# Performance work log

Hardware: AMD Instinct MI355X
Metric: run time of the kernel (lower is better)

The kernel has to match this reference:

```python
import jax, jax.numpy as jnp
import numpy as np

N = 50000        # nodes per node type (user, item)
D_IN = 256       # node_in_dim
D_REL = 64       # rel_in_dim
K = 8            # num_heads
D_OUT = 32       # node_out_dim (per head); K*D_OUT = 256
D_RELOUT = 32    # rel_out_dim (per head)
E = 300000       # edges per relation direction
SLOPE = 0.2

# relations: 0 = user-rates->item, 1 = item-rated-by->user,
#            2 = user-clicks->item, 3 = item-clicked-by->user
STYPE = [0, 1, 0, 1]   # 0=user, 1=item
DTYPE = [1, 0, 1, 0]
REV   = [1, 0, 3, 2]
GROUP = [[0, 2], [1, 3], [0, 2], [1, 3]]  # relations sharing this relation's dtype


def setup_inputs() -> dict:
    key = jax.random.key(0)
    ks = jax.random.split(key, 16)
    feats = jax.random.normal(ks[0], (4, N, D_IN), jnp.float32)
    rel_feats = jax.random.normal(ks[1], (4, D_REL), jnp.float32)
    src_rates = jax.random.randint(ks[2], (E,), 0, N, jnp.int32)
    dst_rates = jax.random.randint(ks[3], (E,), 0, N, jnp.int32)
    src_clicks = jax.random.randint(ks[4], (E,), 0, N, jnp.int32)
    dst_clicks = jax.random.randint(ks[5], (E,), 0, N, jnp.int32)
    s = 0.05
    W_node = s * jax.random.normal(ks[6], (2, D_IN, K * D_OUT), jnp.float32)          # fc_node per ntype (no bias)
    Wr = s * jax.random.normal(ks[7], (4, D_REL, 2 * K * D_OUT), jnp.float32)         # fc_rel per etype (no bias)
    Wres = s * jax.random.normal(ks[8], (2, D_IN, K * D_OUT), jnp.float32)            # fc_res per ntype
    bres = s * jax.random.normal(ks[9], (2, K * D_OUT), jnp.float32)
    resw = jax.random.uniform(ks[10], (2,), jnp.float32)                              # res_weight per ntype
    rel_attn = s * jax.random.normal(ks[11], (4, K, D_OUT), jnp.float32)              # rel_attn per etype
    Wupd = s * jax.random.normal(ks[12], (4, D_REL, K * D_RELOUT), jnp.float32)       # fc_upd per etype
    bupd = s * jax.random.normal(ks[13], (4, K * D_RELOUT), jnp.float32)
    return dict(feats=feats, rel_feats=rel_feats, src_rates=src_rates, dst_rates=dst_rates,
                src_clicks=src_clicks, dst_clicks=dst_clicks, W_node=W_node, Wr=Wr,
                Wres=Wres, bres=bres, resw=resw, rel_attn=rel_attn, Wupd=Wupd, bupd=bupd)


def _leaky(x):
    return jnp.where(x >= 0, x, SLOPE * x)


def _rel_graph_conv(hs, hd, attn, src, dst):
    """GAT-style conv for one relation. hs,hd: (N,K,D_OUT); attn: (K,2*D_OUT)."""
    el = (hs * attn[:, :D_OUT]).sum(-1)                    # (N_src, K)
    er = (hd * attn[:, D_OUT:]).sum(-1)                    # (N_dst, K)
    e = _leaky(el[src] + er[dst])                          # (E, K)
    # edge softmax grouped by destination node
    m = jax.ops.segment_max(e, dst, num_segments=N)        # (N, K)
    m = jnp.where(jnp.isfinite(m), m, 0.0)                 # nodes with no incoming edges
    ex = jnp.exp(e - m[dst])
    z = jax.ops.segment_sum(ex, dst, num_segments=N)
    a = ex / z[dst]                                        # (E, K)
    msg = hs[src] * a[:, :, None]                          # (E, K, D_OUT)
    out = jax.ops.segment_sum(msg, dst, num_segments=N)    # (N, K, D_OUT)
    return jax.nn.relu(out.reshape(N, K * D_OUT))


def reference(feats, rel_feats, src_rates, dst_rates, src_clicks, dst_clicks,
              W_node, Wr, Wres, bres, resw, rel_attn, Wupd, bupd):
    srcs = [src_rates, dst_rates, src_clicks, dst_clicks]
    dsts = [dst_rates, src_rates, dst_clicks, src_clicks]

    node_rel = []
    for r in range(4):
        # feat_src = feats of stype nodes (stored under the reverse relation); feat_dst under r
        hs = (feats[REV[r]] @ W_node[STYPE[r]]).reshape(N, K, D_OUT)
        hd = (feats[r] @ W_node[DTYPE[r]]).reshape(N, K, D_OUT)
        attn = (rel_feats[r] @ Wr[r]).reshape(K, 2 * D_OUT)
        conv = _rel_graph_conv(hs, hd, attn, srcs[r], dsts[r])
        # residual per destination node type
        alpha = jax.nn.sigmoid(resw[DTYPE[r]])
        inherit = feats[r] @ Wres[DTYPE[r]] + bres[DTYPE[r]]
        node_rel.append(alpha * conv + (1.0 - alpha) * inherit)

    # cross-relation attention per relation (over relations sharing the same dtype)
    out_feats = []
    for r in range(4):
        h = jnp.stack([node_rel[i] for i in GROUP[r]], 0).reshape(len(GROUP[r]), N, K, D_OUT)
        scores = (rel_attn[r] * h).sum(-1, keepdims=True)           # (R, N, K, 1)
        w = jax.nn.softmax(_leaky(scores), axis=0)
        out_feats.append((w * h).sum(0).reshape(N, K * D_OUT))
    out_nodes = jnp.stack(out_feats, 0)                             # (4, N, K*D_OUT)

    rel_out = jnp.einsum('rd,rdo->ro', rel_feats, Wupd) + bupd      # (4, K*D_RELOUT)
    return out_nodes, rel_out
```

## Files before the change

### kernel.cpp

```cpp
#include <hip/hip_runtime.h>

typedef unsigned short u16;
typedef __bf16 bf16x8 __attribute__((ext_vector_type(8)));
typedef float f32x4 __attribute__((ext_vector_type(4)));

#define N_NODES 50000
#define N_EDGES 300000
#define NP      12800000
#define NE8     400000

#define WP_OFF    0L
#define ATTN_OFF  524288L
#define ALPHA_OFF 532480L
#define P_OFF     532544L
#define EL_OFF    102932544L
#define ER_OFF    109332544L
#define CNT_OFF   115732544L
#define CUR_OFF   116532544L
#define ROW_OFF   117332544L
#define BS_OFF    118132560L
#define COL_OFF   118135696L

__device__ __forceinline__ float bf2f(u16 u){
  union { unsigned int i; float f; } v; v.i = ((unsigned int)u) << 16; return v.f;
}
__device__ __forceinline__ u16 f2bf(float f){
  union { float f; unsigned int i; } v; v.f = f;
  unsigned int x = v.i;
  x += 0x7fffu + ((x >> 16) & 1u);
  return (u16)(x >> 16);
}
__device__ __forceinline__ float leaky(float x){ return x >= 0.f ? x : 0.2f * x; }

__global__ void small_k(const float* __restrict__ rel_feats, const float* __restrict__ Wr,
                        const float* __restrict__ Wupd, const float* __restrict__ bupd,
                        const float* __restrict__ resw,
                        float* __restrict__ attn, float* __restrict__ alpha,
                        float* __restrict__ out_tail){
  int r = blockIdx.x, t = threadIdx.x;
  for (int j = t; j < 512; j += 256){
    float s = 0.f;
    for (int d = 0; d < 64; ++d)
      s += rel_feats[r*64 + d] * Wr[(r*64 + d)*512 + j];
    attn[r*512 + j] = s;
  }
  {
    float s = 0.f;
    for (int d = 0; d < 64; ++d)
      s += rel_feats[r*64 + d] * Wupd[(r*64 + d)*256 + t];
    out_tail[r*256 + t] = s + bupd[r*256 + t];
  }
  if (r == 0 && t < 2) alpha[t] = 1.f / (1.f + __expf(-resw[t]));
}

__global__ void prepack_k(const float* __restrict__ Wn, const float* __restrict__ Wres,
                          u16* __restrict__ Wp){
  int tid = blockIdx.x*256 + threadIdx.x;
  int m = tid >> 16, rem = tid & 65535;
  int kt = rem >> 13, rem2 = rem & 8191;
  int n = rem2 >> 5, kk = rem2 & 31;
  const float* src = (m < 2) ? (Wn + m*65536) : (Wres + (m - 2)*65536);
  Wp[tid] = f2bf(src[(kt*32 + kk)*256 + n]);
}

__global__ __launch_bounds__(256, 2) void gemm_k(const float* __restrict__ A,
                                              const u16* __restrict__ Wpn, const u16* __restrict__ Wpr,
                                              const float* __restrict__ bias,
                                              const float* __restrict__ alpha_ws, int tix,
                                              u16* __restrict__ Pout, float* __restrict__ out,
                                              const float* __restrict__ attnL, const float* __restrict__ attnR,
                                              float* __restrict__ ELb, float* __restrict__ ERb){
  const int tid = threadIdx.x;
  const int lane = tid & 63, wave = tid >> 6;
  const int quad = lane >> 4, n0 = lane & 15;
  const int wrow = blockIdx.x*64;
  const int cbase = wave*64;
  f32x4 accn[4][4], accr[4][4];
#pragma unroll
  for (int f = 0; f < 4; ++f)
#pragma unroll
    for (int nt = 0; nt < 4; ++nt){
      accn[f][nt] = f32x4{0.f,0.f,0.f,0.f};
      accr[f][nt] = f32x4{0.f,0.f,0.f,0.f};
    }

  for (int kt = 0; kt < 8; ++kt){
    const u16* bpn = Wpn + kt*8192 + (cbase + n0)*32 + quad*8;
    const u16* bpr = Wpr + kt*8192 + (cbase + n0)*32 + quad*8;
    bf16x8 bn[4], br[4];
#pragma unroll
    for (int nt = 0; nt < 4; ++nt){
      bn[nt] = *(const bf16x8*)(bpn + nt*16*32);
      br[nt] = *(const bf16x8*)(bpr + nt*16*32);
    }
    union { bf16x8 v; u16 s[8]; } af[4];
#pragma unroll
    for (int f = 0; f < 4; ++f){
      int row = wrow + f*16 + n0;
      if (row < N_NODES){
        const float* ap = A + (size_t)row*256 + kt*32 + quad*8;
        f32x4 a0 = *(const f32x4*)ap;
        f32x4 a1 = *(const f32x4*)(ap + 4);
#pragma unroll
        for (int j = 0; j < 4; ++j){ af[f].s[j] = f2bf(a0[j]); af[f].s[4+j] = f2bf(a1[j]); }
      } else {
#pragma unroll
        for (int j = 0; j < 8; ++j) af[f].s[j] = 0;
      }
    }
#pragma unroll
    for (int f = 0; f < 4; ++f)
#pragma unroll
      for (int nt = 0; nt < 4; ++nt){
        accn[f][nt] = __builtin_amdgcn_mfma_f32_16x16x32_bf16(af[f].v, bn[nt], accn[f][nt], 0, 0, 0);
        accr[f][nt] = __builtin_amdgcn_mfma_f32_16x16x32_bf16(af[f].v, br[nt], accr[f][nt], 0, 0, 0);
      }
  }

  const float one_m_al = 1.f - alpha_ws[tix];
#pragma unroll
  for (int f = 0; f < 4; ++f)
#pragma unroll
    for (int nt = 0; nt < 4; ++nt){
      int col = cbase + nt*16 + n0;
      float b = bias[col];
#pragma unroll
      for (int reg = 0; reg < 4; ++reg){
        int row = wrow + f*16 + quad*4 + reg;
        if (row < N_NODES){
          out[(size_t)row*256 + col] = one_m_al * (accr[f][nt][reg] + b);
          Pout[(size_t)row*256 + col] = f2bf(accn[f][nt][reg]);
        }
      }
    }

  const int h0 = 2*wave, h1 = 2*wave + 1;
  const float aL00 = attnL[h0*64 + n0], aL01 = attnL[h0*64 + 16 + n0];
  const float aL10 = attnL[h1*64 + n0], aL11 = attnL[h1*64 + 16 + n0];
  const float aR00 = attnR[h0*64 + n0], aR01 = attnR[h0*64 + 16 + n0];
  const float aR10 = attnR[h1*64 + n0], aR11 = attnR[h1*64 + 16 + n0];
#pragma unroll
  for (int f = 0; f < 4; ++f){
#pragma unroll
    for (int reg = 0; reg < 4; ++reg){
      float e0 = accn[f][0][reg]*aL00 + accn[f][1][reg]*aL01;
      float e1 = accn[f][2][reg]*aL10 + accn[f][3][reg]*aL11;
      float r0 = accn[f][0][reg]*aR00 + accn[f][1][reg]*aR01;
      float r1 = accn[f][2][reg]*aR10 + accn[f][3][reg]*aR11;
      e0 += __shfl_xor(e0, 1); e0 += __shfl_xor(e0, 2); e0 += __shfl_xor(e0, 4); e0 += __shfl_xor(e0, 8);
      e1 += __shfl_xor(e1, 1); e1 += __shfl_xor(e1, 2); e1 += __shfl_xor(e1, 4); e1 += __shfl_xor(e1, 8);
      r0 += __shfl_xor(r0, 1); r0 += __shfl_xor(r0, 2); r0 += __shfl_xor(r0, 4); r0 += __shfl_xor(r0, 8);
      r1 += __shfl_xor(r1, 1); r1 += __shfl_xor(r1, 2); r1 += __shfl_xor(r1, 4); r1 += __shfl_xor(r1, 8);
      int row = wrow + f*16 + quad*4 + reg;
      if (row < N_NODES){
        if (n0 == 0)      ELb[row*8 + h0] = e0;
        else if (n0 == 1) ELb[row*8 + h1] = e1;
        else if (n0 == 2) ERb[row*8 + h0] = r0;
        else if (n0 == 3) ERb[row*8 + h1] = r1;
      }
    }
  }
}

__global__ void zero_k(int* __restrict__ p, int n){
  int i = blockIdx.x*256 + threadIdx.x; if (i < n) p[i] = 0;
}
__global__ void hist_k(const int* __restrict__ sr, const int* __restrict__ dr,
                       const int* __restrict__ sc, const int* __restrict__ dc,
                       int* __restrict__ counts){
  int r = blockIdx.y; int e = blockIdx.x*256 + threadIdx.x;
  if (e >= N_EDGES) return;
  const int* dst = (r == 0) ? dr : (r == 1) ? sr : (r == 2) ? dc : sc;
  atomicAdd(&counts[r*N_NODES + dst[e]], 1);
}
__global__ void scan1_k(const int* __restrict__ counts, int* __restrict__ rowptr,
                        int* __restrict__ bsums){
  int r = blockIdx.y; int i = blockIdx.x*256 + threadIdx.x;
  int lane = threadIdx.x & 63, wave = threadIdx.x >> 6;
  int v = (i < N_NODES) ? counts[r*N_NODES + i] : 0;
  int orig = v;
  for (int off = 1; off < 64; off <<= 1){ int t = __shfl_up(v, off); if (lane >= off) v += t; }
  __shared__ int wsum[4];
  if (lane == 63) wsum[wave] = v;
  __syncthreads();
  int add = 0;
  for (int w = 0; w < wave; ++w) add += wsum[w];
  v += add;
  if (i < N_NODES) rowptr[r*(N_NODES+1) + i] = v - orig;
  if (threadIdx.x == 255) bsums[r*196 + blockIdx.x] = v;
}
__global__ void scan2_k(int* __restrict__ bsums){
  int lane = threadIdx.x & 63, r = threadIdx.x >> 6;
  int carry = 0;
  for (int c = 0; c < 4; ++c){
    int i = c*64 + lane;
    int v = (i < 196) ? bsums[r*196 + i] : 0;
    int orig = v;
    for (int off = 1; off < 64; off <<= 1){ int t = __shfl_up(v, off); if (lane >= off) v += t; }
    int excl = v - orig + carry;
    if (i < 196) bsums[r*196 + i] = excl;
    carry += __shfl(v, 63);
  }
}
__global__ void scan3_k(const int* __restrict__ bsums, int* __restrict__ rowptr){
  int r = blockIdx.y; int i = blockIdx.x*256 + threadIdx.x;
  if (i < N_NODES) rowptr[r*(N_NODES+1) + i] += bsums[r*196 + blockIdx.x];
  if (i == N_NODES) rowptr[r*(N_NODES+1) + N_NODES] = N_EDGES;
}
__global__ void scatter_k(const int* __restrict__ sr, const int* __restrict__ dr,
                          const int* __restrict__ sc, const int* __restrict__ dc,
                          const int* __restrict__ rowptr, int* __restrict__ cur,
                          int* __restrict__ colsrc){
  int r = blockIdx.y; int e = blockIdx.x*256 + threadIdx.x;
  if (e >= N_EDGES) return;
  const int* dst = (r == 0) ? dr : (r == 1) ? sr : (r == 2) ? dc : sc;
  const int* src = (r == 0) ? sr : (r == 1) ? dr : (r == 2) ? sc : dc;
  int d = dst[e];
  int pos = rowptr[r*(N_NODES+1) + d] + atomicAdd(&cur[r*N_NODES + d], 1);
  colsrc[r*N_EDGES + pos] = src[e];
}

__global__ __launch_bounds__(256) void aggcross_k(
    const int* __restrict__ rowptr, const int* __restrict__ colsrc,
    const float* __restrict__ EL, const float* __restrict__ ER,
    const u16* __restrict__ P, const float* __restrict__ rel_attn,
    const float* __restrict__ alpha_ws, float* __restrict__ out){
  const int g = blockIdx.y;
  const int wave = threadIdx.x >> 6, lane = threadIdx.x & 63;
  const int n = blockIdx.x*4 + wave;
  if (n >= N_NODES) return;
  const int k0 = lane >> 3, j = lane & 7;
  const float al = alpha_ws[g ^ 1];
  f32x4 h[2];
#pragma unroll
  for (int which = 0; which < 2; ++which){
    const int r = g + which*2;
    const int rp0 = rowptr[r*(N_NODES+1) + n], rp1 = rowptr[r*(N_NODES+1) + n + 1];
    const float er = ER[(size_t)r*NE8 + n*8 + k0];
    const float* el = EL + (size_t)r*NE8;
    const int* cs = colsrc + r*N_EDGES;
    const u16* Ps = P + (size_t)(r ^ 1)*NP;

    float z = 0.f, a0 = 0.f, a1 = 0.f, a2 = 0.f, a3 = 0.f;
    for (int base = rp0; base < rp1; base += 8){
      const int cnt = rp1 - base;
      const int m = cnt < 8 ? cnt : 8;
      int sj = cs[base + (j < m ? j : 0)];
      float x = leaky(el[sj*8 + k0] + er);
      float p = (j < m) ? __expf(x - 10.f) : 0.f;
      ushort4 hv[8]; float pv[8];
#pragma unroll
      for (int t = 0; t < 8; ++t){
        if (t < m){
          int s = __shfl(sj, t);
          hv[t] = *(const ushort4*)(Ps + (size_t)s*256 + lane*4);
          pv[t] = __shfl(p, (lane & 56) | t);
        }
      }
#pragma unroll
      for (int t = 0; t < 8; ++t){
        if (t < m){
          float q = pv[t];
          z += q;
          a0 += q*bf2f(hv[t].x); a1 += q*bf2f(hv[t].y);
          a2 += q*bf2f(hv[t].z); a3 += q*bf2f(hv[t].w);
        }
      }
    }
    float inv = (rp1 > rp0) ? 1.f / z : 0.f;
    f32x4 inh = *(const f32x4*)(out + (size_t)r*NP + (size_t)n*256 + lane*4);
    h[which][0] = al * fmaxf(a0*inv, 0.f) + inh[0];
    h[which][1] = al * fmaxf(a1*inv, 0.f) + inh[1];
    h[which][2] = al * fmaxf(a2*inv, 0.f) + inh[2];
    h[which][3] = al * fmaxf(a3*inv, 0.f) + inh[3];
  }
#pragma unroll
  for (int which = 0; which < 2; ++which){
    int rr = g + which*2;
    const float* ra = rel_attn + rr*256 + k0*32 + j*4;
    float s0 = 0.f, s1 = 0.f;
#pragma unroll
    for (int jj = 0; jj < 4; ++jj){
      float a = ra[jj];
      s0 += a * h[0][jj]; s1 += a * h[1][jj];
    }
    s0 += __shfl_xor(s0, 1); s1 += __shfl_xor(s1, 1);
    s0 += __shfl_xor(s0, 2); s1 += __shfl_xor(s1, 2);
    s0 += __shfl_xor(s0, 4); s1 += __shfl_xor(s1, 4);
    float l0 = leaky(s0), l1 = leaky(s1);
    float mx = fmaxf(l0, l1);
    float e0 = __expf(l0 - mx), e1 = __expf(l1 - mx);
    float w0 = e0 / (e0 + e1), w1 = 1.f - w0;
    f32x4 o;
#pragma unroll
    for (int jj = 0; jj < 4; ++jj) o[jj] = w0*h[0][jj] + w1*h[1][jj];
    *(f32x4*)(out + ((size_t)rr*N_NODES + n)*256 + lane*4) = o;
  }
}

extern "C" void kernel_launch(void* const* d_in, const int* in_sizes, int n_in,
                              void* d_out, int out_size, void* d_ws, size_t ws_size,
                              hipStream_t stream) {
  (void)in_sizes; (void)n_in; (void)out_size; (void)ws_size;
  const float* feats      = (const float*)d_in[0];
  const float* rel_feats  = (const float*)d_in[1];
  const int*   src_rates  = (const int*)d_in[2];
  const int*   dst_rates  = (const int*)d_in[3];
  const int*   src_clicks = (const int*)d_in[4];
  const int*   dst_clicks = (const int*)d_in[5];
  const float* W_node     = (const float*)d_in[6];
  const float* Wr         = (const float*)d_in[7];
  const float* Wres       = (const float*)d_in[8];
  const float* bres       = (const float*)d_in[9];
  const float* resw       = (const float*)d_in[10];
  const float* rel_attn   = (const float*)d_in[11];
  const float* Wupd       = (const float*)d_in[12];
  const float* bupd       = (const float*)d_in[13];

  char* w = (char*)d_ws;
  u16*   Wp     = (u16*)(w + WP_OFF);
  float* attn   = (float*)(w + ATTN_OFF);
  float* alpha  = (float*)(w + ALPHA_OFF);
  u16*   P      = (u16*)(w + P_OFF);
  float* EL     = (float*)(w + EL_OFF);
  float* ER     = (float*)(w + ER_OFF);
  int*   counts = (int*)(w + CNT_OFF);
  int*   cur    = (int*)(w + CUR_OFF);
  int*   rowptr = (int*)(w + ROW_OFF);
  int*   bsums  = (int*)(w + BS_OFF);
  int*   colsrc = (int*)(w + COL_OFF);
  float* out    = (float*)d_out;

  static const int DT[4] = {1, 0, 1, 0};

  zero_k<<<1563, 256, 0, stream>>>(counts, 400000);
  small_k<<<4, 256, 0, stream>>>(rel_feats, Wr, Wupd, bupd, resw, attn, alpha,
                                 out + (size_t)4*NP);
  prepack_k<<<1024, 256, 0, stream>>>(W_node, Wres, Wp);

  hist_k<<<dim3(1172, 4), 256, 0, stream>>>(src_rates, dst_rates, src_clicks, dst_clicks, counts);
  scan1_k<<<dim3(196, 4), 256, 0, stream>>>(counts, rowptr, bsums);
  scan2_k<<<1, 256, 0, stream>>>(bsums);
  scan3_k<<<dim3(196, 4), 256, 0, stream>>>(bsums, rowptr);
  scatter_k<<<dim3(1172, 4), 256, 0, stream>>>(src_rates, dst_rates, src_clicks, dst_clicks,
                                               rowptr, cur, colsrc);

  for (int i = 0; i < 4; ++i)
    gemm_k<<<782, 256, 0, stream>>>(feats + (size_t)i*NP,
                                    Wp + DT[i]*65536, Wp + (2 + DT[i])*65536,
                                    bres + DT[i]*256, alpha, DT[i],
                                    P + (size_t)i*NP, out + (size_t)i*NP,
                                    attn + (i ^ 1)*512, attn + i*512 + 32,
                                    EL + (size_t)(i ^ 1)*NE8, ER + (size_t)i*NE8);

  aggcross_k<<<dim3(12500, 2), 256, 0, stream>>>(rowptr, colsrc, EL, ER, P,
                                                 rel_attn, alpha, out);
}
```

Baseline: 927.0 us.

## Merge per-relation GEMM launches into one grid and software-pipeline global loads

Replaces four separate gemm_k launches with one launch over a 2D grid, where blockIdx.y selects the relation and the kernel derives the weight, bias, attention and output pointers itself. Inside the K loop, the A rows and packed weight fragments for the next k-tile are prefetched into registers before the current tile's MFMAs, and the loop is fully unrolled. This aims to hide global load latency and cut launch gaps and tail effects between relations. The extra live registers could lower occupancy under the 256x2 launch bounds.

Result: slower. 1.713 ms (+84.8%).

```diff
diff --git a/kernel.cpp b/kernel.cpp
--- a/kernel.cpp
+++ b/kernel.cpp
@@ -32,6 +32,8 @@
 }
 __device__ __forceinline__ float leaky(float x){ return x >= 0.f ? x : 0.2f * x; }
 
+union AFu { bf16x8 v; u16 s[8]; };
+
 __global__ void small_k(const float* __restrict__ rel_feats, const float* __restrict__ Wr,
                         const float* __restrict__ Wupd, const float* __restrict__ bupd,
                         const float* __restrict__ resw,
@@ -63,13 +65,26 @@
   Wp[tid] = f2bf(src[(kt*32 + kk)*256 + n]);
 }
 
-__global__ __launch_bounds__(256, 2) void gemm_k(const float* __restrict__ A,
-                                              const u16* __restrict__ Wpn, const u16* __restrict__ Wpr,
-                                              const float* __restrict__ bias,
-                                              const float* __restrict__ alpha_ws, int tix,
-                                              u16* __restrict__ Pout, float* __restrict__ out,
-                                              const float* __restrict__ attnL, const float* __restrict__ attnR,
-                                              float* __restrict__ ELb, float* __restrict__ ERb){
+__global__ __launch_bounds__(256, 2) void gemm_k(const float* __restrict__ feats,
+                                              const u16* __restrict__ Wp,
+                                              const float* __restrict__ bres,
+                                              const float* __restrict__ alpha_ws,
+                                              u16* __restrict__ Pbase, float* __restrict__ outbase,
+                                              const float* __restrict__ attn,
+                                              float* __restrict__ EL, float* __restrict__ ER){
+  const int rel = blockIdx.y;
+  const int dt = 1 - (rel & 1);
+  const float* __restrict__ A     = feats + (size_t)rel*NP;
+  const u16*   __restrict__ Wpn   = Wp + dt*65536;
+  const u16*   __restrict__ Wpr   = Wp + (2 + dt)*65536;
+  const float* __restrict__ bias  = bres + dt*256;
+  const float* __restrict__ attnL = attn + (rel ^ 1)*512;
+  const float* __restrict__ attnR = attn + rel*512 + 32;
+  u16*   __restrict__ Pout = Pbase + (size_t)rel*NP;
+  float* __restrict__ out  = outbase + (size_t)rel*NP;
+  float* __restrict__ ELb  = EL + (size_t)(rel ^ 1)*NE8;
+  float* __restrict__ ERb  = ER + (size_t)rel*NE8;
+
   const int tid = threadIdx.x;
   const int lane = tid & 63, wave = tid >> 6;
   const int quad = lane >> 4, n0 = lane & 15;
@@ -84,28 +99,47 @@
       accr[f][nt] = f32x4{0.f,0.f,0.f,0.f};
     }
 
+  f32x4 ra0[4], ra1[4];
+  bf16x8 bn[4], br[4];
+#pragma unroll
+  for (int f = 0; f < 4; ++f){
+    int row = wrow + f*16 + n0;
+    if (row < N_NODES){
+      const float* ap = A + (size_t)row*256 + quad*8;
+      ra0[f] = *(const f32x4*)ap;
+      ra1[f] = *(const f32x4*)(ap + 4);
+    } else {
+      ra0[f] = f32x4{0.f,0.f,0.f,0.f};
+      ra1[f] = f32x4{0.f,0.f,0.f,0.f};
+    }
+  }
+  {
+    const u16* bpn = Wpn + (cbase + n0)*32 + quad*8;
+    const u16* bpr = Wpr + (cbase + n0)*32 + quad*8;
+#pragma unroll
+    for (int nt = 0; nt < 4; ++nt){
+      bn[nt] = *(const bf16x8*)(bpn + nt*512);
+      br[nt] = *(const bf16x8*)(bpr + nt*512);
+    }
+  }
+
+#pragma unroll
   for (int kt = 0; kt < 8; ++kt){
-    const u16* bpn = Wpn + kt*8192 + (cbase + n0)*32 + quad*8;
-    const u16* bpr = Wpr + kt*8192 + (cbase + n0)*32 + quad*8;
-    bf16x8 bn[4], br[4];
-#pragma unroll
-    for (int nt = 0; nt < 4; ++nt){
-      bn[nt] = *(const bf16x8*)(bpn + nt*16*32);
-      br[nt] = *(const bf16x8*)(bpr + nt*16*32);
-    }
-    union { bf16x8 v; u16 s[8]; } af[4];
+    AFu af[4];
 #pragma unroll
     for (int f = 0; f < 4; ++f){
-      int row = wrow + f*16 + n0;
-      if (row < N_NODES){
-        const float* ap = A + (size_t)row*256 + kt*32 + quad*8;
-        f32x4 a0 = *(const f32x4*)ap;
-        f32x4 a1 = *(const f32x4*)(ap + 4);
-#pragma unroll
-        for (int j = 0; j < 4; ++j){ af[f].s[j] = f2bf(a0[j]); af[f].s[4+j] = f2bf(a1[j]); }
-      } else {
-#pragma unroll
-        for (int j = 0; j < 8; ++j) af[f].s[j] = 0;
+#pragma unroll
+      for (int j = 0; j < 4; ++j){ af[f].s[j] = f2bf(ra0[f][j]); af[f].s[4+j] = f2bf(ra1[f][j]); }
+    }
+    if (kt < 7){
+#pragma unroll
+      for (int f = 0; f < 4; ++f){
+        int row = wrow + f*16 + n0;
+        if (row < N_NODES){
+          const float* ap = A + (size_t)row*256 + (kt+1)*32 + quad*8;
+          ra0[f] = *(const f32x4*)ap;
+          ra1[f] = *(const f32x4*)(ap + 4);
+        }
       }
     }
 #pragma unroll
@@ -115,9 +149,18 @@
         accn[f][nt] = __builtin_amdgcn_mfma_f32_16x16x32_bf16(af[f].v, bn[nt], accn[f][nt], 0, 0, 0);
         accr[f][nt] = __builtin_amdgcn_mfma_f32_16x16x32_bf16(af[f].v, br[nt], accr[f][nt], 0, 0, 0);
       }
-  }
-
-  const float one_m_al = 1.f - alpha_ws[tix];
+    if (kt < 7){
+      const u16* bpn = Wpn + (kt+1)*8192 + (cbase + n0)*32 + quad*8;
+      const u16* bpr = Wpr + (kt+1)*8192 + (cbase + n0)*32 + quad*8;
+#pragma unroll
+      for (int nt = 0; nt < 4; ++nt){
+        bn[nt] = *(const bf16x8*)(bpn + nt*512);
+        br[nt] = *(const bf16x8*)(bpr + nt*512);
+      }
+    }
+  }
+
+  const float one_m_al = 1.f - alpha_ws[dt];
 #pragma unroll
   for (int f = 0; f < 4; ++f)
 #pragma unroll
@@ -331,8 +374,6 @@
   int*   colsrc = (int*)(w + COL_OFF);
   float* out    = (float*)d_out;
 
-  static const int DT[4] = {1, 0, 1, 0};
-
   zero_k<<<1563, 256, 0, stream>>>(counts, 400000);
   small_k<<<4, 256, 0, stream>>>(rel_feats, Wr, Wupd, bupd, resw, attn, alpha,
                                  out + (size_t)4*NP);
@@ -345,13 +386,7 @@
   scatter_k<<<dim3(1172, 4), 256, 0, stream>>>(src_rates, dst_rates, src_clicks, dst_clicks,
                                                rowptr, cur, colsrc);
 
-  for (int i = 0; i < 4; ++i)
-    gemm_k<<<782, 256, 0, stream>>>(feats + (size_t)i*NP,
-                                    Wp + DT[i]*65536, Wp + (2 + DT[i])*65536,
-                                    bres + DT[i]*256, alpha, DT[i],
-                                    P + (size_t)i*NP, out + (size_t)i*NP,
-                                    attn + (i ^ 1)*512, attn + i*512 + 32,
-                                    EL + (size_t)(i ^ 1)*NE8, ER + (size_t)i*NE8);
+  gemm_k<<<dim3(782, 4), 256, 0, stream>>>(feats, Wp, bres, alpha, P, out, attn, EL, ER);
 
   aggcross_k<<<dim3(12500, 2), 256, 0, stream>>>(rowptr, colsrc, EL, ER, P,
                                                  rel_attn, alpha, out);
```

## Split GEMM into per-matrix blocks and merge four launches into one grid

Applied to the files above, without the earlier changes.

The fused GEMM that computed both the node projection and the residual projection in one block is split so each block computes only one of them (blockIdx.y selects relation and matrix). This halves the accumulator registers and allows launch bounds of 4 blocks per CU, and the four per-relation launches become a single 782x8 grid. The cost is that the A tile (fp32 features plus the bf16 conversion) is now loaded and converted twice, once per matrix, which doubles input reads.

New measurement: 928.3 us. No clear change (+0.1%).

```diff
diff --git a/kernel.cpp b/kernel.cpp
--- a/kernel.cpp
+++ b/kernel.cpp
@@ -63,37 +63,38 @@
   Wp[tid] = f2bf(src[(kt*32 + kk)*256 + n]);
 }
 
-__global__ __launch_bounds__(256, 2) void gemm_k(const float* __restrict__ A,
-                                              const u16* __restrict__ Wpn, const u16* __restrict__ Wpr,
-                                              const float* __restrict__ bias,
-                                              const float* __restrict__ alpha_ws, int tix,
-                                              u16* __restrict__ Pout, float* __restrict__ out,
-                                              const float* __restrict__ attnL, const float* __restrict__ attnR,
-                                              float* __restrict__ ELb, float* __restrict__ ERb){
+__global__ __launch_bounds__(256, 4) void gemm_k(const float* __restrict__ feats,
+                                              const u16* __restrict__ Wp,
+                                              const float* __restrict__ bres,
+                                              const float* __restrict__ alpha_ws,
+                                              u16* __restrict__ Pbase, float* __restrict__ outbase,
+                                              const float* __restrict__ attn,
+                                              float* __restrict__ EL, float* __restrict__ ER){
+  const int rel = blockIdx.y >> 1;
+  const int mat = blockIdx.y & 1;
+  const int dt = 1 - (rel & 1);
+  const float* __restrict__ A = feats + (size_t)rel*NP;
+  const u16*   __restrict__ W = Wp + (mat*2 + dt)*65536;
+
   const int tid = threadIdx.x;
   const int lane = tid & 63, wave = tid >> 6;
   const int quad = lane >> 4, n0 = lane & 15;
   const int wrow = blockIdx.x*64;
   const int cbase = wave*64;
-  f32x4 accn[4][4], accr[4][4];
+  f32x4 acc[4][4];
 #pragma unroll
   for (int f = 0; f < 4; ++f)
 #pragma unroll
-    for (int nt = 0; nt < 4; ++nt){
-      accn[f][nt] = f32x4{0.f,0.f,0.f,0.f};
-      accr[f][nt] = f32x4{0.f,0.f,0.f,0.f};
-    }
+    for (int nt = 0; nt < 4; ++nt)
+      acc[f][nt] = f32x4{0.f,0.f,0.f,0.f};
 
   for (int kt = 0; kt < 8; ++kt){
-    const u16* bpn = Wpn + kt*8192 + (cbase + n0)*32 + quad*8;
-    const u16* bpr = Wpr + kt*8192 + (cbase + n0)*32 + quad*8;
-    bf16x8 bn[4], br[4];
-#pragma unroll
-    for (int nt = 0; nt < 4; ++nt){
-      bn[nt] = *(const bf16x8*)(bpn + nt*16*32);
-      br[nt] = *(const bf16x8*)(bpr + nt*16*32);
-    }
-    union { bf16x8 v; u16 s[8]; } af[4];
+    const u16* bp = W + kt*8192 + (cbase + n0)*32 + quad*8;
+    bf16x8 b[4];
+#pragma unroll
+    for (int nt = 0; nt < 4; ++nt)
+      b[nt] = *(const bf16x8*)(bp + nt*512);
+    bf16x8 af[4];
 #pragma unroll
     for (int f = 0; f < 4; ++f){
       int row = wrow + f*16 + n0;
@@ -102,38 +103,57 @@
         f32x4 a0 = *(const f32x4*)ap;
         f32x4 a1 = *(const f32x4*)(ap + 4);
 #pragma unroll
-        for (int j = 0; j < 4; ++j){ af[f].s[j] = f2bf(a0[j]); af[f].s[4+j] = f2bf(a1[j]); }
+        for (int j = 0; j < 4; ++j){ af[f][j] = (__bf16)a0[j]; af[f][4+j] = (__bf16)a1[j]; }
       } else {
 #pragma unroll
-        for (int j = 0; j < 8; ++j) af[f].s[j] = 0;
+        for (int j = 0; j < 8; ++j) af[f][j] = (__bf16)0.f;
       }
     }
 #pragma unroll
     for (int f = 0; f < 4; ++f)
 #pragma unroll
+      for (int nt = 0; nt < 4; ++nt)
+        acc[f][nt] = __builtin_amdgcn_mfma_f32_16x16x32_bf16(af[f], b[nt], acc[f][nt], 0, 0, 0);
+  }
+
+  if (mat == 1){
+    float* __restrict__ out = outbase + (size_t)rel*NP;
+    const float* __restrict__ bias = bres + dt*256;
+    const float one_m_al = 1.f - alpha_ws[dt];
+#pragma unroll
+    for (int f = 0; f < 4; ++f)
+#pragma unroll
       for (int nt = 0; nt < 4; ++nt){
-        accn[f][nt] = __builtin_amdgcn_mfma_f32_16x16x32_bf16(af[f].v, bn[nt], accn[f][nt], 0, 0, 0);
-        accr[f][nt] = __builtin_amdgcn_mfma_f32_16x16x32_bf16(af[f].v, br[nt], accr[f][nt], 0, 0, 0);
-      }
-  }
-
-  const float one_m_al = 1.f - alpha_ws[tix];
+        int col = cbase + nt*16 + n0;
+        float bv = bias[col];
+#pragma unroll
+        for (int reg = 0; reg < 4; ++reg){
+          int row = wrow + f*16 + quad*4 + reg;
+          if (row < N_NODES)
+            out[(size_t)row*256 + col] = one_m_al * (acc[f][nt][reg] + bv);
+        }
+      }
+    return;
+  }
+
+  u16* __restrict__ Pout = Pbase + (size_t)rel*NP;
 #pragma unroll
   for (int f = 0; f < 4; ++f)
 #pragma unroll
     for (int nt = 0; nt < 4; ++nt){
       int col = cbase + nt*16 + n0;
-      float b = bias[col];
 #pragma unroll
       for (int reg = 0; reg < 4; ++reg){
         int row = wrow + f*16 + quad*4 + reg;
-        if (row < N_NODES){
-          out[(size_t)row*256 + col] = one_m_al * (accr[f][nt][reg] + b);
-          Pout[(size_t)row*256 + col] = f2bf(accn[f][nt][reg]);
-        }
-      }
-    }
-
+        if (row < N_NODES)
+          Pout[(size_t)row*256 + col] = f2bf(acc[f][nt][reg]);
+      }
+    }
+
+  const float* __restrict__ attnL = attn + (rel ^ 1)*512;
+  const float* __restrict__ attnR = attn + rel*512 + 32;
+  float* __restrict__ ELb = EL + (size_t)(rel ^ 1)*NE8;
+  float* __restrict__ ERb = ER + (size_t)rel*NE8;
   const int h0 = 2*wave, h1 = 2*wave + 1;
   const float aL00 = attnL[h0*64 + n0], aL01 = attnL[h0*64 + 16 + n0];
   const float aL10 = attnL[h1*64 + n0], aL11 = attnL[h1*64 + 16 + n0];
@@ -143,10 +163,10 @@
   for (int f = 0; f < 4; ++f){
 #pragma unroll
     for (int reg = 0; reg < 4; ++reg){
-      float e0 = accn[f][0][reg]*aL00 + accn[f][1][reg]*aL01;
-      float e1 = accn[f][2][reg]*aL10 + accn[f][3][reg]*aL11;
-      float r0 = accn[f][0][reg]*aR00 + accn[f][1][reg]*aR01;
-      float r1 = accn[f][2][reg]*aR10 + accn[f][3][reg]*aR11;
+      float e0 = acc[f][0][reg]*aL00 + acc[f][1][reg]*aL01;
+      float e1 = acc[f][2][reg]*aL10 + acc[f][3][reg]*aL11;
+      float r0 = acc[f][0][reg]*aR00 + acc[f][1][reg]*aR01;
+      float r1 = acc[f][2][reg]*aR10 + acc[f][3][reg]*aR11;
       e0 += __shfl_xor(e0, 1); e0 += __shfl_xor(e0, 2); e0 += __shfl_xor(e0, 4); e0 += __shfl_xor(e0, 8);
       e1 += __shfl_xor(e1, 1); e1 += __shfl_xor(e1, 2); e1 += __shfl_xor(e1, 4); e1 += __shfl_xor(e1, 8);
       r0 += __shfl_xor(r0, 1); r0 += __shfl_xor(r0, 2); r0 += __shfl_xor(r0, 4); r0 += __shfl_xor(r0, 8);
@@ -331,8 +351,6 @@
   int*   colsrc = (int*)(w + COL_OFF);
   float* out    = (float*)d_out;
 
-  static const int DT[4] = {1, 0, 1, 0};
-
   zero_k<<<1563, 256, 0, stream>>>(counts, 400000);
   small_k<<<4, 256, 0, stream>>>(rel_feats, Wr, Wupd, bupd, resw, attn, alpha,
                                  out + (size_t)4*NP);
@@ -345,13 +363,7 @@
   scatter_k<<<dim3(1172, 4), 256, 0, stream>>>(src_rates, dst_rates, src_clicks, dst_clicks,
                                                rowptr, cur, colsrc);
 
-  for (int i = 0; i < 4; ++i)
-    gemm_k<<<782, 256, 0, stream>>>(feats + (size_t)i*NP,
-                                    Wp + DT[i]*65536, Wp + (2 + DT[i])*65536,
-                                    bres + DT[i]*256, alpha, DT[i],
-                                    P + (size_t)i*NP, out + (size_t)i*NP,
-                                    attn + (i ^ 1)*512, attn + i*512 + 32,
-                                    EL + (size_t)(i ^ 1)*NE8, ER + (size_t)i*NE8);
+  gemm_k<<<dim3(782, 8), 256, 0, stream>>>(feats, Wp, bres, alpha, P, out, attn, EL, ER);
 
   aggcross_k<<<dim3(12500, 2), 256, 0, stream>>>(rowptr, colsrc, EL, ER, P,
                                                  rel_attn, alpha, out);
```
